# Kernel optimization log

Measured on AMD Instinct MI355X. Metric: run time of the kernel, lower is better.

## Reference

```python
import jax, jax.numpy as jnp
import numpy as np

HEADS = 16
D_MODEL = 1024
D_K = D_MODEL // HEADS
BATCH = 4
SEQ = 1024
NEG_BIG = -1000000000.0


def setup_inputs() -> dict:
    key = jax.random.key(0)
    ks = jax.random.split(key, 7)
    s = 1.0 / np.sqrt(D_MODEL)
    return {
        "q": jax.random.normal(ks[0], (BATCH, SEQ, D_MODEL), jnp.float32),
        "k": jax.random.normal(ks[1], (BATCH, SEQ, D_MODEL), jnp.float32),
        "v": jax.random.normal(ks[2], (BATCH, SEQ, D_MODEL), jnp.float32),
        "Wq": jax.random.normal(ks[3], (D_MODEL, D_MODEL), jnp.float32) * s,
        "Wk": jax.random.normal(ks[4], (D_MODEL, D_MODEL), jnp.float32) * s,
        "Wv": jax.random.normal(ks[5], (D_MODEL, D_MODEL), jnp.float32) * s,
        "Wo": jax.random.normal(ks[6], (D_MODEL, D_MODEL), jnp.float32) * s,
    }


def reference(q, k, v, Wq, Wk, Wv, Wo):
    bs = q.shape[0]
    residual = q
    # torch Linear(bias=False): x @ W.T ; then the module's quirky reshape
    # view(bs, h, -1, d_k) on the contiguous [bs, seq, d_model] buffer.
    qh = (q @ Wq.T).reshape(bs, HEADS, -1, D_K)   # [b, h, s, d_k]
    kh = (k @ Wk.T).reshape(bs, HEADS, -1, D_K)
    vh = (v @ Wv.T).reshape(bs, HEADS, -1, D_K)
    scores = jnp.einsum("bhqd,bhkd->bhqk", qh, kh) / jnp.sqrt(
        jnp.asarray(D_K, qh.dtype))
    # data-dependent mask: exact-zero scores get -1e9 before softmax
    scores = jnp.where(scores == 0, jnp.asarray(NEG_BIG, scores.dtype), scores)
    attn = jax.nn.softmax(scores, axis=-1)  # dropout is identity in eval mode
    out = jnp.einsum("bhqk,bhkd->bhqd", attn, vh)  # [b, h, s, d_k]
    concat = jnp.swapaxes(out, 1, 2).reshape(bs, -1, D_MODEL)
    return concat @ Wo.T + residual
```

## Files before the change

### kernel.cpp

```cpp
#include <hip/hip_runtime.h>
#include <stdint.h>

typedef __bf16 bf16x8 __attribute__((ext_vector_type(8)));
typedef __bf16 bf16x2v __attribute__((ext_vector_type(2)));
typedef float f32x4 __attribute__((ext_vector_type(4)));
typedef uint16_t u16x8 __attribute__((ext_vector_type(8)));
typedef uint16_t u16x4 __attribute__((ext_vector_type(4)));
typedef uint32_t u32x2 __attribute__((ext_vector_type(2)));
typedef short s16x4 __attribute__((ext_vector_type(4)));

#define DMODEL 1024
#define K1SC 0.1803368801111244f

__device__ __forceinline__ uint16_t bfc(float f) {
  __bf16 h = (__bf16)f;
  return __builtin_bit_cast(uint16_t, h);
}
__device__ __forceinline__ uint32_t pk32(float a, float b) {
  bf16x2v t = {(__bf16)a, (__bf16)b};
  return __builtin_bit_cast(uint32_t, t);
}
__device__ __forceinline__ void gld16(const void* src, void* dst) {
  __builtin_amdgcn_global_load_lds((const __attribute__((address_space(1))) void*)src,
                                   (__attribute__((address_space(3))) void*)dst, 16, 0, 0);
}

__global__ void cvt_all_kernel(const float* __restrict__ q, const float* __restrict__ k,
                               const float* __restrict__ v, const float* __restrict__ Wq,
                               const float* __restrict__ Wk, const float* __restrict__ Wv,
                               const float* __restrict__ Wo, uint16_t* __restrict__ qb,
                               uint16_t* __restrict__ kb, uint16_t* __restrict__ vb,
                               uint16_t* __restrict__ Wqb, uint16_t* __restrict__ Wkb,
                               uint16_t* __restrict__ Wvb, uint16_t* __restrict__ Wob) {
  int bid = blockIdx.x;
  const float* src;
  uint16_t* dst;
  int off;
  if (bid < 12288) {
    int s = bid >> 12;
    src = s == 0 ? q : (s == 1 ? k : v);
    dst = s == 0 ? qb : (s == 1 ? kb : vb);
    off = bid & 4095;
  } else {
    int r = bid - 12288;
    int s = r >> 10;
    src = s == 0 ? Wq : (s == 1 ? Wk : (s == 2 ? Wv : Wo));
    dst = s == 0 ? Wqb : (s == 1 ? Wkb : (s == 2 ? Wvb : Wob));
    off = r & 1023;
  }
  int i = off * 256 + threadIdx.x;
  f32x4 x = ((const f32x4*)src)[i];
  u16x4 r;
#pragma unroll
  for (int j = 0; j < 4; ++j) r[j] = bfc(x[j]);
  ((u16x4*)dst)[i] = r;
}

__global__ __launch_bounds__(256, 2)
void gemm_qkv_kernel(const uint16_t* __restrict__ A0, const uint16_t* __restrict__ A1,
                     const uint16_t* __restrict__ A2, const uint16_t* __restrict__ W0,
                     const uint16_t* __restrict__ W1, const uint16_t* __restrict__ W2,
                     uint16_t* __restrict__ C0, uint16_t* __restrict__ C1,
                     uint16_t* __restrict__ C2) {
  int orig = blockIdx.x;
  int lin = (orig & 7) * 96 + (orig >> 3);
  int z = lin >> 8;
  int rem = lin & 255;
  int m0 = (rem >> 3) * 128, n0 = (rem & 7) * 128;

  const uint16_t* A = z == 0 ? A0 : (z == 1 ? A1 : A2);
  const uint16_t* Bw = z == 0 ? W0 : (z == 1 ? W1 : W2);
  uint16_t* C = z == 0 ? C0 : (z == 1 ? C1 : C2);
  const float osc = (z == 0) ? K1SC : 1.0f;

  __shared__ __align__(16) uint16_t As[2][128 * 32];
  __shared__ __align__(16) uint16_t Bs[2][128 * 32];
  const int t = threadIdx.x;
  const int lane = t & 63;
  const int w = t >> 6;
  const int wr = w >> 1, wc = w & 1;
  const int lr = lane & 15, ksl = lane >> 4;
  const int sw2 = (lr & 3) << 4;

  f32x4 acc[4][4];
#pragma unroll
  for (int m = 0; m < 4; ++m)
#pragma unroll
    for (int n = 0; n < 4; ++n) acc[m][n] = (f32x4){0.f, 0.f, 0.f, 0.f};

  auto stage = [&](int buf, int k0) {
#pragma unroll
    for (int cc = 0; cc < 2; ++cc) {
      int idx = cc * 256 + t;
      int row = idx >> 2, ch = idx & 3;
      int so = ((ch * 16) ^ ((row & 3) << 4)) >> 1;
      gld16(A + (size_t)(m0 + row) * DMODEL + k0 + so, &As[buf][idx * 8]);
    }
#pragma unroll
    for (int cc = 0; cc < 2; ++cc) {
      int idx = cc * 256 + t;
      int row = idx >> 2, ch = idx & 3;
      int so = ((ch * 16) ^ ((row & 3) << 4)) >> 1;
      gld16(Bw + (size_t)(n0 + row) * DMODEL + k0 + so, &Bs[buf][idx * 8]);
    }
  };

  stage(0, 0);
  __syncthreads();

  int cur = 0;
#pragma unroll 1
  for (int kt = 0; kt < 32; ++kt) {
    if (kt < 31) stage(cur ^ 1, (kt + 1) * 32);
    const char* Ab = (const char*)&As[cur][0];
    const char* Bb = (const char*)&Bs[cur][0];
    const int co = (ksl * 16) ^ sw2;
    bf16x8 af[4], bfv[4];
#pragma unroll
    for (int m = 0; m < 4; ++m)
      af[m] = *(const bf16x8*)(Ab + (wr * 64 + m * 16 + lr) * 64 + co);
#pragma unroll
    for (int n = 0; n < 4; ++n)
      bfv[n] = *(const bf16x8*)(Bb + (wc * 64 + n * 16 + lr) * 64 + co);
    __builtin_amdgcn_s_setprio(1);
#pragma unroll
    for (int m = 0; m < 4; ++m)
#pragma unroll
      for (int n = 0; n < 4; ++n)
        acc[m][n] = __builtin_amdgcn_mfma_f32_16x16x32_bf16(af[m], bfv[n], acc[m][n], 0, 0, 0);
    __builtin_amdgcn_s_setprio(0);
    __syncthreads();
    cur ^= 1;
  }

#pragma unroll
  for (int m = 0; m < 4; ++m) {
#pragma unroll
    for (int n = 0; n < 4; ++n) {
      int col = n0 + wc * 64 + n * 16 + lr;
#pragma unroll
      for (int r = 0; r < 4; ++r) {
        int row = m0 + wr * 64 + m * 16 + ksl * 4 + r;
        C[(size_t)row * DMODEL + col] = bfc(acc[m][n][r] * osc);
      }
    }
  }
}

__global__ __launch_bounds__(256, 2)
void gemm_o_kernel(const uint16_t* __restrict__ A, const uint16_t* __restrict__ Bw,
                   float* __restrict__ Cf, const float* __restrict__ resid) {
  int orig = blockIdx.x;
  int lin = (orig & 7) * 64 + (orig >> 3);
  int m0 = (lin >> 3) * 64, n0 = (lin & 7) * 128;

  __shared__ __align__(16) uint16_t As[2][64 * 32];
  __shared__ __align__(16) uint16_t Bs[2][128 * 32];
  const int t = threadIdx.x;
  const int lane = t & 63;
  const int w = t >> 6;
  const int wr = w >> 1, wc = w & 1;
  const int lr = lane & 15, ksl = lane >> 4;
  const int sw2 = (lr & 3) << 4;

  f32x4 acc[2][4];
#pragma unroll
  for (int m = 0; m < 2; ++m)
#pragma unroll
    for (int n = 0; n < 4; ++n) acc[m][n] = (f32x4){0.f, 0.f, 0.f, 0.f};

  auto stage = [&](int buf, int k0) {
    {
      int row = t >> 2, ch = t & 3;
      int so = ((ch * 16) ^ ((row & 3) << 4)) >> 1;
      gld16(A + (size_t)(m0 + row) * DMODEL + k0 + so, &As[buf][t * 8]);
    }
#pragma unroll
    for (int cc = 0; cc < 2; ++cc) {
      int idx = cc * 256 + t;
      int row = idx >> 2, ch = idx & 3;
      int so = ((ch * 16) ^ ((row & 3) << 4)) >> 1;
      gld16(Bw + (size_t)(n0 + row) * DMODEL + k0 + so, &Bs[buf][idx * 8]);
    }
  };

  stage(0, 0);
  __syncthreads();

  int cur = 0;
#pragma unroll 1
  for (int kt = 0; kt < 32; ++kt) {
    if (kt < 31) stage(cur ^ 1, (kt + 1) * 32);
    const char* Ab = (const char*)&As[cur][0];
    const char* Bb = (const char*)&Bs[cur][0];
    const int co = (ksl * 16) ^ sw2;
    bf16x8 af[2], bfv[4];
#pragma unroll
    for (int m = 0; m < 2; ++m)
      af[m] = *(const bf16x8*)(Ab + (wr * 32 + m * 16 + lr) * 64 + co);
#pragma unroll
    for (int n = 0; n < 4; ++n)
      bfv[n] = *(const bf16x8*)(Bb + (wc * 64 + n * 16 + lr) * 64 + co);
    __builtin_amdgcn_s_setprio(1);
#pragma unroll
    for (int m = 0; m < 2; ++m)
#pragma unroll
      for (int n = 0; n < 4; ++n)
        acc[m][n] = __builtin_amdgcn_mfma_f32_16x16x32_bf16(af[m], bfv[n], acc[m][n], 0, 0, 0);
    __builtin_amdgcn_s_setprio(0);
    __syncthreads();
    cur ^= 1;
  }

#pragma unroll
  for (int m = 0; m < 2; ++m) {
#pragma unroll
    for (int n = 0; n < 4; ++n) {
      int col = n0 + wc * 64 + n * 16 + lr;
#pragma unroll
      for (int r = 0; r < 4; ++r) {
        int row = m0 + wr * 32 + m * 16 + ksl * 4 + r;
        size_t idx = (size_t)row * DMODEL + col;
        Cf[idx] = acc[m][n][r] + resid[idx];
      }
    }
  }
}

__global__ __launch_bounds__(256, 4)
void attn_mfma_kernel(const uint16_t* __restrict__ Pq, const uint16_t* __restrict__ Pk,
                      const uint16_t* __restrict__ Pv, uint16_t* __restrict__ Cc) {
  __shared__ __align__(16) uint16_t Ks[2][64 * 64];
  __shared__ __align__(16) uint16_t Vts[2][64 * 64];

  const int t = threadIdx.x;
  const int w = t >> 6;
  const int lane = t & 63;
  const int lr = lane & 15;
  const int ksl = lane >> 4;
  int orig = blockIdx.x;
  int lin = (orig & 7) * 128 + (orig >> 3);
  const int bh = lin >> 4, qt = lin & 15;
  const int b = bh >> 4, h = bh & 15;

  const uint16_t* Qb = Pq + (size_t)bh * 65536 + (size_t)qt * 4096;
  const uint16_t* Kb = Pk + (size_t)bh * 65536;
  const uint16_t* Vb = Pv + (size_t)bh * 65536;

  bf16x8 qf0, qf1;
  {
    const uint16_t* qrow = Qb + (size_t)(w * 16 + lr) * 64 + ksl * 8;
    qf0 = *(const bf16x8*)(qrow);
    qf1 = *(const bf16x8*)(qrow + 32);
  }

  f32x4 Oa[4];
#pragma unroll
  for (int n = 0; n < 4; ++n) Oa[n] = (f32x4){0.f, 0.f, 0.f, 0.f};
  f32x4 lsum4 = {0.f, 0.f, 0.f, 0.f};

  const int sw = (lr & 7) << 4;
  const int p2 = t & 31;
  const int c8 = t >> 5;

  int qko[4][2], pvo[4][4], wvo[8];
#pragma unroll
  for (int n = 0; n < 4; ++n) {
#pragma unroll
    for (int c = 0; c < 2; ++c) qko[n][c] = (n * 16 + lr) * 128 + ((c * 64 + ksl * 16) ^ sw);
#pragma unroll
    for (int nd = 0; nd < 4; ++nd) pvo[n][nd] = (nd * 16 + lr) * 128 + ((n * 32 + ksl * 8) ^ sw);
  }
#pragma unroll
  for (int i = 0; i < 8; ++i) {
    int d = c8 * 8 + i;
    wvo[i] = d * 128 + ((p2 * 4) ^ ((d & 7) << 4));
  }

  const int sr0 = t >> 3;
  const int sc0 = (((t & 7) * 16) ^ ((sr0 & 7) << 4)) >> 1;
  const uint16_t* srcK = Kb + (size_t)sr0 * 64 + sc0;
  const uint16_t* srcV = Vb + (size_t)(p2 * 2) * 64 + c8 * 8;
  const int kd0 = t * 16, kd1 = (256 + t) * 16;

  char* kb0 = (char*)&Ks[0][0];
  char* kb1 = (char*)&Ks[1][0];
  char* vb0 = (char*)&Vts[0][0];
  char* vb1 = (char*)&Vts[1][0];

  u16x8 va, vb2;
  auto stageK = [&](char* kbuf) {
    gld16(srcK, kbuf + kd0);
    gld16(srcK + 2048, kbuf + kd1);
  };
  auto loadV = [&]() {
    va = *(const u16x8*)srcV;
    vb2 = *(const u16x8*)(srcV + 64);
  };
  auto writeV = [&](char* vbuf) {
#pragma unroll
    for (int i = 0; i < 8; ++i) {
      uint32_t val = (uint32_t)va[i] | ((uint32_t)vb2[i] << 16);
      *(uint32_t*)(vbuf + wvo[i]) = val;
    }
  };

  stageK(kb0);
  loadV();
  writeV(vb0);
  __syncthreads();

  const char* kcur = kb0; char* knx = kb1;
  const char* vcur = vb0; char* vnx = vb1;

#pragma unroll 1
  for (int kt = 0; kt < 16; ++kt) {
    if (kt < 15) { srcK += 4096; stageK(knx); srcV += 4096; loadV(); }

    f32x4 S[4];
#pragma unroll
    for (int n = 0; n < 4; ++n) S[n] = (f32x4){0.f, 0.f, 0.f, 0.f};
    __builtin_amdgcn_s_setprio(1);
#pragma unroll
    for (int n = 0; n < 4; ++n) {
      bf16x8 kf0 = *(const bf16x8*)(kcur + qko[n][0]);
      bf16x8 kf1 = *(const bf16x8*)(kcur + qko[n][1]);
      S[n] = __builtin_amdgcn_mfma_f32_16x16x32_bf16(kf0, qf0, S[n], 0, 0, 0);
      S[n] = __builtin_amdgcn_mfma_f32_16x16x32_bf16(kf1, qf1, S[n], 0, 0, 0);
    }
    __builtin_amdgcn_s_setprio(0);

    f32x4 psum = {0.f, 0.f, 0.f, 0.f};
    f32x4 p4[4];
#pragma unroll
    for (int n = 0; n < 4; ++n) {
#pragma unroll
      for (int r = 0; r < 4; ++r) {
        float x = S[n][r];
        float e = __builtin_amdgcn_exp2f(x);
        p4[n][r] = (x == 0.f) ? 0.f : e;
      }
      psum += p4[n];
    }
    lsum4 += psum;

    __builtin_amdgcn_s_setprio(1);
#pragma unroll
    for (int n = 0; n < 4; ++n) {
      u32x2 pa32 = {pk32(p4[n][0], p4[n][1]), pk32(p4[n][2], p4[n][3])};
      s16x4 pa = __builtin_bit_cast(s16x4, pa32);
#pragma unroll
      for (int nd = 0; nd < 4; ++nd) {
        s16x4 vf = *(const s16x4*)(vcur + pvo[n][nd]);
        Oa[nd] = __builtin_amdgcn_mfma_f32_16x16x16bf16_1k(pa, vf, Oa[nd], 0, 0, 0);
      }
    }
    __builtin_amdgcn_s_setprio(0);

    if (kt < 15) writeV(vnx);
    __syncthreads();
    const char* tk = kcur; kcur = knx; knx = (char*)tk;
    const char* tv = vcur; vcur = vnx; vnx = (char*)tv;
  }

  float lrow = (lsum4[0] + lsum4[1]) + (lsum4[2] + lsum4[3]);
  lrow += __shfl_xor(lrow, 16);
  lrow += __shfl_xor(lrow, 32);
  f32x4 inv4;
#pragma unroll
  for (int r = 0; r < 4; ++r) inv4[r] = 1.f / __shfl(lrow, ksl * 4 + r);

  uint16_t* dst = Cc + (size_t)b * 1048576 + (size_t)(qt * 64 + w * 16) * 1024 + h * 64;
#pragma unroll
  for (int r = 0; r < 4; ++r) {
    int qq = ksl * 4 + r;
#pragma unroll
    for (int n = 0; n < 4; ++n) {
      dst[qq * 1024 + n * 16 + lr] = bfc(Oa[n][r] * inv4[r]);
    }
  }
}

extern "C" void kernel_launch(void* const* d_in, const int* in_sizes, int n_in,
                              void* d_out, int out_size, void* d_ws, size_t ws_size,
                              hipStream_t stream) {
  const float* q  = (const float*)d_in[0];
  const float* k  = (const float*)d_in[1];
  const float* v  = (const float*)d_in[2];
  const float* Wq = (const float*)d_in[3];
  const float* Wk = (const float*)d_in[4];
  const float* Wv = (const float*)d_in[5];
  const float* Wo = (const float*)d_in[6];
  float* out = (float*)d_out;
  char* ws = (char*)d_ws;
  const size_t MB = 1u << 20;
  uint16_t* qb  = (uint16_t*)(ws + 0 * MB);
  uint16_t* kb  = (uint16_t*)(ws + 8 * MB);
  uint16_t* vb  = (uint16_t*)(ws + 16 * MB);
  uint16_t* Wqb = (uint16_t*)(ws + 24 * MB);
  uint16_t* Wkb = (uint16_t*)(ws + 26 * MB);
  uint16_t* Wvb = (uint16_t*)(ws + 28 * MB);
  uint16_t* Wob = (uint16_t*)(ws + 30 * MB);
  uint16_t* Pq  = (uint16_t*)(ws + 32 * MB);
  uint16_t* Pk  = (uint16_t*)(ws + 40 * MB);
  uint16_t* Pv  = (uint16_t*)(ws + 48 * MB);
  uint16_t* Cc  = (uint16_t*)(ws + 56 * MB);

  cvt_all_kernel<<<16384, 256, 0, stream>>>(q, k, v, Wq, Wk, Wv, Wo,
                                            qb, kb, vb, Wqb, Wkb, Wvb, Wob);

  gemm_qkv_kernel<<<768, 256, 0, stream>>>(qb, kb, vb, Wqb, Wkb, Wvb,
                                           Pq, Pk, Pv);

  attn_mfma_kernel<<<1024, 256, 0, stream>>>(Pq, Pk, Pv, Cc);

  gemm_o_kernel<<<512, 256, 0, stream>>>(Cc, Wob, out, q);
}
```

Baseline: 105.2 us.

## Fuse fp32-to-bf16 activation conversion into QKV projection GEMM A-tile load

Drops the separate conversion of q/k/v activations to bf16. The QKV GEMM now stages fp32 A tiles straight into LDS with an XOR swizzle and converts them to bf16 in registers before the MFMAs. This removes a full read and write pass over 48 MB of activations and one kernel's worth of traffic, while only the weights are still pre-converted. In exchange LDS use for A doubles and each k-step does extra conversion work and larger LDS reads, which may lower occupancy or lengthen the inner loop.

```diff
diff --git a/kernel.cpp b/kernel.cpp
--- a/kernel.cpp
+++ b/kernel.cpp
@@ -25,30 +25,15 @@
                                    (__attribute__((address_space(3))) void*)dst, 16, 0, 0);
 }
 
-__global__ void cvt_all_kernel(const float* __restrict__ q, const float* __restrict__ k,
-                               const float* __restrict__ v, const float* __restrict__ Wq,
-                               const float* __restrict__ Wk, const float* __restrict__ Wv,
-                               const float* __restrict__ Wo, uint16_t* __restrict__ qb,
-                               uint16_t* __restrict__ kb, uint16_t* __restrict__ vb,
-                               uint16_t* __restrict__ Wqb, uint16_t* __restrict__ Wkb,
-                               uint16_t* __restrict__ Wvb, uint16_t* __restrict__ Wob) {
+__global__ void cvt_w_kernel(const float* __restrict__ Wq, const float* __restrict__ Wk,
+                             const float* __restrict__ Wv, const float* __restrict__ Wo,
+                             uint16_t* __restrict__ Wqb, uint16_t* __restrict__ Wkb,
+                             uint16_t* __restrict__ Wvb, uint16_t* __restrict__ Wob) {
   int bid = blockIdx.x;
-  const float* src;
-  uint16_t* dst;
-  int off;
-  if (bid < 12288) {
-    int s = bid >> 12;
-    src = s == 0 ? q : (s == 1 ? k : v);
-    dst = s == 0 ? qb : (s == 1 ? kb : vb);
-    off = bid & 4095;
-  } else {
-    int r = bid - 12288;
-    int s = r >> 10;
-    src = s == 0 ? Wq : (s == 1 ? Wk : (s == 2 ? Wv : Wo));
-    dst = s == 0 ? Wqb : (s == 1 ? Wkb : (s == 2 ? Wvb : Wob));
-    off = r & 1023;
-  }
-  int i = off * 256 + threadIdx.x;
+  int s = bid >> 10;
+  const float* src = s == 0 ? Wq : (s == 1 ? Wk : (s == 2 ? Wv : Wo));
+  uint16_t* dst = s == 0 ? Wqb : (s == 1 ? Wkb : (s == 2 ? Wvb : Wob));
+  int i = (bid & 1023) * 256 + threadIdx.x;
   f32x4 x = ((const f32x4*)src)[i];
   u16x4 r;
 #pragma unroll
@@ -57,44 +42,36 @@
 }
 
 __global__ __launch_bounds__(256, 2)
-void gemm_qkv_kernel(const uint16_t* __restrict__ A0, const uint16_t* __restrict__ A1,
-                     const uint16_t* __restrict__ A2, const uint16_t* __restrict__ W0,
+void gemm_qkv_kernel(const float* __restrict__ A0, const float* __restrict__ A1,
+                     const float* __restrict__ A2, const uint16_t* __restrict__ W0,
                      const uint16_t* __restrict__ W1, const uint16_t* __restrict__ W2,
                      uint16_t* __restrict__ C0, uint16_t* __restrict__ C1,
                      uint16_t* __restrict__ C2) {
   int orig = blockIdx.x;
   int lin = (orig & 7) * 96 + (orig >> 3);
-  int z = lin >> 8;
-  int rem = lin & 255;
+  int z = lin >> 8, rem = lin & 255;
   int m0 = (rem >> 3) * 128, n0 = (rem & 7) * 128;
 
-  const uint16_t* A = z == 0 ? A0 : (z == 1 ? A1 : A2);
+  const float* A = z == 0 ? A0 : (z == 1 ? A1 : A2);
   const uint16_t* Bw = z == 0 ? W0 : (z == 1 ? W1 : W2);
   uint16_t* C = z == 0 ? C0 : (z == 1 ? C1 : C2);
   const float osc = (z == 0) ? K1SC : 1.0f;
 
-  __shared__ __align__(16) uint16_t As[2][128 * 32];
+  __shared__ __align__(16) char As[2][128 * 128];
   __shared__ __align__(16) uint16_t Bs[2][128 * 32];
   const int t = threadIdx.x;
   const int lane = t & 63;
   const int w = t >> 6;
   const int wr = w >> 1, wc = w & 1;
   const int lr = lane & 15, ksl = lane >> 4;
-  const int sw2 = (lr & 3) << 4;
-
-  f32x4 acc[4][4];
-#pragma unroll
-  for (int m = 0; m < 4; ++m)
-#pragma unroll
-    for (int n = 0; n < 4; ++n) acc[m][n] = (f32x4){0.f, 0.f, 0.f, 0.f};
 
   auto stage = [&](int buf, int k0) {
 #pragma unroll
-    for (int cc = 0; cc < 2; ++cc) {
+    for (int cc = 0; cc < 4; ++cc) {
       int idx = cc * 256 + t;
-      int row = idx >> 2, ch = idx & 3;
-      int so = ((ch * 16) ^ ((row & 3) << 4)) >> 1;
-      gld16(A + (size_t)(m0 + row) * DMODEL + k0 + so, &As[buf][idx * 8]);
+      int row = idx >> 3, ch = idx & 7;
+      int sc = (ch ^ (row & 7)) * 4;
+      gld16(A + (size_t)(m0 + row) * DMODEL + k0 + sc, &As[buf][idx * 16]);
     }
 #pragma unroll
     for (int cc = 0; cc < 2; ++cc) {
@@ -105,20 +82,37 @@
     }
   };
 
+  f32x4 acc[4][4];
+#pragma unroll
+  for (int m = 0; m < 4; ++m)
+#pragma unroll
+    for (int n = 0; n < 4; ++n) acc[m][n] = (f32x4){0.f, 0.f, 0.f, 0.f};
+
   stage(0, 0);
   __syncthreads();
+
+  const int rs = lr & 7;
+  const int aoff0 = ((2 * ksl) ^ rs) * 16;
+  const int aoff1 = ((2 * ksl + 1) ^ rs) * 16;
+  const int co = (ksl ^ (lr & 3)) * 16;
 
   int cur = 0;
 #pragma unroll 1
   for (int kt = 0; kt < 32; ++kt) {
     if (kt < 31) stage(cur ^ 1, (kt + 1) * 32);
-    const char* Ab = (const char*)&As[cur][0];
+    const char* Ab = &As[cur][0];
     const char* Bb = (const char*)&Bs[cur][0];
-    const int co = (ksl * 16) ^ sw2;
     bf16x8 af[4], bfv[4];
 #pragma unroll
-    for (int m = 0; m < 4; ++m)
-      af[m] = *(const bf16x8*)(Ab + (wr * 64 + m * 16 + lr) * 64 + co);
+    for (int m = 0; m < 4; ++m) {
+      const char* rp = Ab + (wr * 64 + m * 16 + lr) * 128;
+      f32x4 lo = *(const f32x4*)(rp + aoff0);
+      f32x4 hi = *(const f32x4*)(rp + aoff1);
+      u16x8 u;
+#pragma unroll
+      for (int j = 0; j < 4; ++j) { u[j] = bfc(lo[j]); u[4 + j] = bfc(hi[j]); }
+      af[m] = __builtin_bit_cast(bf16x8, u);
+    }
 #pragma unroll
     for (int n = 0; n < 4; ++n)
       bfv[n] = *(const bf16x8*)(Bb + (wc * 64 + n * 16 + lr) * 64 + co);
@@ -394,23 +388,18 @@
   float* out = (float*)d_out;
   char* ws = (char*)d_ws;
   const size_t MB = 1u << 20;
-  uint16_t* qb  = (uint16_t*)(ws + 0 * MB);
-  uint16_t* kb  = (uint16_t*)(ws + 8 * MB);
-  uint16_t* vb  = (uint16_t*)(ws + 16 * MB);
-  uint16_t* Wqb = (uint16_t*)(ws + 24 * MB);
-  uint16_t* Wkb = (uint16_t*)(ws + 26 * MB);
-  uint16_t* Wvb = (uint16_t*)(ws + 28 * MB);
-  uint16_t* Wob = (uint16_t*)(ws + 30 * MB);
-  uint16_t* Pq  = (uint16_t*)(ws + 32 * MB);
-  uint16_t* Pk  = (uint16_t*)(ws + 40 * MB);
-  uint16_t* Pv  = (uint16_t*)(ws + 48 * MB);
-  uint16_t* Cc  = (uint16_t*)(ws + 56 * MB);
-
-  cvt_all_kernel<<<16384, 256, 0, stream>>>(q, k, v, Wq, Wk, Wv, Wo,
-                                            qb, kb, vb, Wqb, Wkb, Wvb, Wob);
-
-  gemm_qkv_kernel<<<768, 256, 0, stream>>>(qb, kb, vb, Wqb, Wkb, Wvb,
-                                           Pq, Pk, Pv);
+  uint16_t* Pq  = (uint16_t*)(ws + 0 * MB);
+  uint16_t* Pk  = (uint16_t*)(ws + 8 * MB);
+  uint16_t* Pv  = (uint16_t*)(ws + 16 * MB);
+  uint16_t* Cc  = (uint16_t*)(ws + 24 * MB);
+  uint16_t* Wqb = (uint16_t*)(ws + 32 * MB);
+  uint16_t* Wkb = (uint16_t*)(ws + 34 * MB);
+  uint16_t* Wvb = (uint16_t*)(ws + 36 * MB);
+  uint16_t* Wob = (uint16_t*)(ws + 38 * MB);
+
+  cvt_w_kernel<<<4096, 256, 0, stream>>>(Wq, Wk, Wv, Wo, Wqb, Wkb, Wvb, Wob);
+
+  gemm_qkv_kernel<<<768, 256, 0, stream>>>(q, k, v, Wqb, Wkb, Wvb, Pq, Pk, Pv);
 
   attn_mfma_kernel<<<1024, 256, 0, stream>>>(Pq, Pk, Pv, Cc);
 
```

Result: faster. 99.35 us (median of 2 runs) (-5.6%).
